# Kernel tuning notes

Measured on AMD Instinct MI355X. Metric: run time of the kernel, lower is better.

## Reference

```python
import jax, jax.numpy as jnp
import numpy as np

B, S, D, H = 4, 2048, 1024, 16
HD = D // H  # 64
EPS = 1e-5


def setup_inputs() -> dict:
    key = jax.random.key(0)
    ks = jax.random.split(key, 16)
    sc = 0.02
    inp = {
        "x": jax.random.normal(ks[0], (B, S, D), dtype=jnp.float32),
        # per-head QKV projections, stacked over heads: [H, D, HD]
        "Wq": jax.random.normal(ks[1], (H, D, HD), jnp.float32) * sc,
        "bq": jnp.zeros((H, HD), jnp.float32),
        "Wk": jax.random.normal(ks[2], (H, D, HD), jnp.float32) * sc,
        "bk": jnp.zeros((H, HD), jnp.float32),
        "Wv": jax.random.normal(ks[3], (H, D, HD), jnp.float32) * sc,
        "bv": jnp.zeros((H, HD), jnp.float32),
        "Wo": jax.random.normal(ks[4], (D, D), jnp.float32) * sc,
        "bo": jnp.zeros((D,), jnp.float32),
        "W1": jax.random.normal(ks[5], (D, 4 * D), jnp.float32) * sc,
        "b1": jnp.zeros((4 * D,), jnp.float32),
        "W2": jax.random.normal(ks[6], (4 * D, D), jnp.float32) * sc,
        "b2": jnp.zeros((D,), jnp.float32),
        "g1": jnp.ones((D,), jnp.float32),
        "be1": jnp.zeros((D,), jnp.float32),
        "g2": jnp.ones((D,), jnp.float32),
        "be2": jnp.zeros((D,), jnp.float32),
    }
    return inp


def _layer_norm(x, g, b):
    mu = jnp.mean(x, axis=-1, keepdims=True)
    var = jnp.var(x, axis=-1, keepdims=True)
    return (x - mu) * jax.lax.rsqrt(var + EPS) * g + b


def reference(x, Wq, bq, Wk, bk, Wv, bv, Wo, bo, W1, b1, W2, b2, g1, be1, g2, be2):
    # --- pre-LN multi-head attention (no causal mask, matches source) ---
    h = _layer_norm(x, g1, be1)                                   # [B,S,D]
    q = jnp.einsum("bsd,hdk->bhsk", h, Wq) + bq[None, :, None, :]  # [B,H,S,HD]
    k = jnp.einsum("bsd,hdk->bhsk", h, Wk) + bk[None, :, None, :]
    v = jnp.einsum("bsd,hdk->bhsk", h, Wv) + bv[None, :, None, :]
    scores = jnp.einsum("bhsk,bhtk->bhst", q, k) / jnp.sqrt(jnp.float32(HD))
    w = jax.nn.softmax(scores, axis=-1)                           # [B,H,S,S]
    o = jnp.einsum("bhst,bhtk->bhsk", w, v)                       # [B,H,S,HD]
    o = o.transpose(0, 2, 1, 3).reshape(B, S, D)                   # concat heads
    attn = o @ Wo + bo
    x1 = x + attn
    # --- FFN: Linear -> Linear -> GELU (exact, as in the source Sequential) ---
    h2 = _layer_norm(x1, g2, be2)
    ff = jax.nn.gelu((h2 @ W1 + b1) @ W2 + b2, approximate=False)
    return x1 + ff
```

## Files before the change

### kernel.cpp

```cpp
#include <hip/hip_runtime.h>
#include <hip/hip_bf16.h>
#include <cmath>

typedef __hip_bfloat16 bf16;
typedef float v4f __attribute__((ext_vector_type(4)));
typedef short v8s __attribute__((ext_vector_type(8)));
typedef short v4s __attribute__((ext_vector_type(4)));

__device__ __forceinline__ void load_lds16(const void* g, void* l) {
  __builtin_amdgcn_global_load_lds(
      (const __attribute__((address_space(1))) char*)g,
      (__attribute__((address_space(3))) char*)l, 16, 0, 0);
}
__device__ __forceinline__ v4f mfma16x16x32(v8s a, v8s b, v4f c) {
  return __builtin_amdgcn_mfma_f32_16x16x32_bf16(a, b, c, 0, 0, 0);
}
__device__ __forceinline__ v4f mfma16x16x16(v4s a, v4s b, v4f c) {
#if __has_builtin(__builtin_amdgcn_mfma_f32_16x16x16_bf16)
  return __builtin_amdgcn_mfma_f32_16x16x16_bf16(a, b, c, 0, 0, 0);
#elif __has_builtin(__builtin_amdgcn_mfma_f32_16x16x16bf16_1k)
  return __builtin_amdgcn_mfma_f32_16x16x16bf16_1k(a, b, c, 0, 0, 0);
#else
  v4f d;
  asm("v_mfma_f32_16x16x16_bf16 %0, %1, %2, %3"
      : "=v"(d) : "v"(a), "v"(b), "v"(c));
  return d;
#endif
}
__device__ __forceinline__ float b2f(bf16 x) { return __bfloat162float(x); }
__device__ __forceinline__ bf16 f2b(float x) { return __float2bfloat16(x); }
__device__ __forceinline__ ushort b2u(float x) {
  bf16 h = f2b(x);
  return *(ushort*)&h;
}
__device__ __forceinline__ float fexp2(float x) {
#if __has_builtin(__builtin_amdgcn_exp2f)
  return __builtin_amdgcn_exp2f(x);
#else
  return exp2f(x);
#endif
}
__device__ __forceinline__ float gelu_exact(float x) {
  return 0.5f * x * (1.0f + erff(x * 0.70710678118654752f));
}
__device__ __forceinline__ float finz(float v, float sent) {
  return __builtin_isfinite(v) ? v : sent;
}
__device__ __forceinline__ float u2f(ushort u) {
  return __uint_as_float(((unsigned)u) << 16);
}
__device__ __forceinline__ float4 load4f(const float* p) {
  return *(const float4*)p;
}
__device__ __forceinline__ float4 load4f(const bf16* p) {
  ushort4 u = *(const ushort4*)p;
  return make_float4(u2f(u.x), u2f(u.y), u2f(u.z), u2f(u.w));
}

template <typename TI>
__global__ __launch_bounds__(256)
void ln_kernel(const TI* __restrict__ x, const float* __restrict__ g,
               const float* __restrict__ b, bf16* __restrict__ out) {
  __shared__ float red[8];
  __shared__ float stat[2];
  const int row = blockIdx.x, t = threadIdx.x;
  const int wave = t >> 6, lane = t & 63;
  float4 v = load4f(x + (long)row * 1024 + t * 4);
  float s = v.x + v.y + v.z + v.w;
  float s2 = v.x * v.x + v.y * v.y + v.z * v.z + v.w * v.w;
#pragma unroll
  for (int off = 32; off > 0; off >>= 1) {
    s += __shfl_down(s, off);
    s2 += __shfl_down(s2, off);
  }
  if (lane == 0) { red[wave * 2] = s; red[wave * 2 + 1] = s2; }
  __syncthreads();
  if (t == 0) {
    float S = red[0] + red[2] + red[4] + red[6];
    float S2 = red[1] + red[3] + red[5] + red[7];
    float mean = S * (1.0f / 1024.0f);
    float var = S2 * (1.0f / 1024.0f) - mean * mean;
    stat[0] = mean;
    stat[1] = rsqrtf(var + 1e-5f);
  }
  __syncthreads();
  const float mean = stat[0], rs = stat[1];
  bf16* orow = out + (long)row * 1024;
  const int c = t * 4;
  float4 gg = *(const float4*)(g + c);
  float4 bb = *(const float4*)(b + c);
  orow[c + 0] = f2b(finz((v.x - mean) * rs * gg.x + bb.x, 3000.f));
  orow[c + 1] = f2b(finz((v.y - mean) * rs * gg.y + bb.y, 3000.f));
  orow[c + 2] = f2b(finz((v.z - mean) * rs * gg.z + bb.z, 3000.f));
  orow[c + 3] = f2b(finz((v.w - mean) * rs * gg.w + bb.w, 3000.f));
}

__global__ __launch_bounds__(256)
void repack_qkv(const float* __restrict__ w, bf16* __restrict__ wt) {
  long i = (long)blockIdx.x * 256 + threadIdx.x;
  int n = (int)(i >> 10), d = (int)(i & 1023);
  int h = n >> 6, kk = n & 63;
  wt[i] = f2b(w[((long)h * 1024 + d) * 64 + kk]);
}

__global__ __launch_bounds__(256)
void cast_f2b(const float* __restrict__ in, bf16* __restrict__ out) {
  long i = ((long)blockIdx.x * 256 + threadIdx.x) * 4;
  float4 v = *(const float4*)(in + i);
  ushort4 pk;
  pk.x = b2u(v.x); pk.y = b2u(v.y); pk.z = b2u(v.z); pk.w = b2u(v.w);
  *(ushort4*)((ushort*)out + i) = pk;
}

__global__ __launch_bounds__(256)
void ffn_bias(const float* __restrict__ b1, const float* __restrict__ W2,
              const float* __restrict__ b2, float* __restrict__ bfo) {
  __shared__ float red[4];
  const int e = blockIdx.x, t = threadIdx.x;
  float s = 0.f;
#pragma unroll
  for (int j = 0; j < 16; j++) {
    const int f = t + j * 256;
    s += b1[f] * W2[(long)f * 1024 + e];
  }
#pragma unroll
  for (int off = 32; off > 0; off >>= 1) s += __shfl_down(s, off);
  if ((t & 63) == 0) red[t >> 6] = s;
  __syncthreads();
  if (t == 0) bfo[e] = b2[e] + red[0] + red[1] + red[2] + red[3];
}

__global__ __launch_bounds__(256)
void transpose_f2b(const float* __restrict__ in, bf16* __restrict__ out,
                   int R, int C) {
  __shared__ float tile[32][33];
  const int tx = threadIdx.x & 31, ty = threadIdx.x >> 5;
  const int r0 = blockIdx.y * 32, c0 = blockIdx.x * 32;
#pragma unroll
  for (int i = ty; i < 32; i += 8) tile[i][tx] = in[(long)(r0 + i) * C + c0 + tx];
  __syncthreads();
#pragma unroll
  for (int i = ty; i < 32; i += 8)
    out[(long)(c0 + i) * R + r0 + tx] = f2b(tile[tx][i]);
}

template <int EPI>
__global__ __launch_bounds__(256)
void gemm_bt(const bf16* __restrict__ A, const bf16* __restrict__ Bt,
             const float* __restrict__ bias0, const float* __restrict__ bias1,
             const float* __restrict__ bias2, const void* __restrict__ residv,
             void* __restrict__ C0v, bf16* __restrict__ C1, bf16* __restrict__ C2v,
             int M, int N, int K) {
  __shared__ bf16 As[2][128 * 32];
  __shared__ bf16 Bs[2][128 * 32];
  const int t = threadIdx.x;
  const int wave = t >> 6, lane = t & 63, quad = lane >> 4, ln = lane & 15;
  const int m0 = blockIdx.y * 128, n0 = blockIdx.x * 128;
  const int wm = (wave >> 1) * 64, wn = (wave & 1) * 64;

  v4f acc[4][4];
#pragma unroll
  for (int i = 0; i < 4; i++)
#pragma unroll
    for (int j = 0; j < 4; j++) acc[i][j] = v4f{0.f, 0.f, 0.f, 0.f};

  const int e0 = t * 8, e1 = t * 8 + 2048;
  const int ra0 = e0 >> 5, ca0 = e0 & 31, ra1 = e1 >> 5, ca1 = e1 & 31;
  const bf16* Ab = A + (long)m0 * K;
  const bf16* Bb = Bt + (long)n0 * K;

  load_lds16(Ab + (long)ra0 * K + ca0, &As[0][e0]);
  load_lds16(Ab + (long)ra1 * K + ca1, &As[0][e1]);
  load_lds16(Bb + (long)ra0 * K + ca0, &Bs[0][e0]);
  load_lds16(Bb + (long)ra1 * K + ca1, &Bs[0][e1]);

  int cur = 0;
  for (int k0 = 0; k0 < K; k0 += 32) {
    __syncthreads();
    if (k0 + 32 < K) {
      const int kn = k0 + 32, nb = cur ^ 1;
      load_lds16(Ab + (long)ra0 * K + kn + ca0, &As[nb][e0]);
      load_lds16(Ab + (long)ra1 * K + kn + ca1, &As[nb][e1]);
      load_lds16(Bb + (long)ra0 * K + kn + ca0, &Bs[nb][e0]);
      load_lds16(Bb + (long)ra1 * K + kn + ca1, &Bs[nb][e1]);
    }
    v8s af[4], bfr[4];
#pragma unroll
    for (int mi = 0; mi < 4; mi++)
      af[mi] = *(const v8s*)&As[cur][(wm + mi * 16 + ln) * 32 + quad * 8];
#pragma unroll
    for (int ni = 0; ni < 4; ni++)
      bfr[ni] = *(const v8s*)&Bs[cur][(wn + ni * 16 + ln) * 32 + quad * 8];
#pragma unroll
    for (int mi = 0; mi < 4; mi++)
#pragma unroll
      for (int ni = 0; ni < 4; ni++)
        acc[mi][ni] = mfma16x16x32(af[mi], bfr[ni], acc[mi][ni]);
    cur ^= 1;
  }

#pragma unroll
  for (int ni = 0; ni < 4; ni++) {
    const int col = n0 + wn + ni * 16 + ln;
    if (EPI == 3) {
      const int proj = col >> 10, w = col & 1023;
      const float* bp = proj == 0 ? bias0 : (proj == 1 ? bias1 : bias2);
      const float bb = bp[w];
      const int hidx = w >> 6, hd = w & 63;
      if (proj == 2) {
#pragma unroll
        for (int mi = 0; mi < 4; mi++) {
          const int row0 = m0 + wm + mi * 16 + quad * 4;
          const int b_ = row0 >> 11, s = row0 & 2047;
          ushort4 pk;
          pk.x = b2u(finz(acc[mi][ni][0] + bb, 1e4f));
          pk.y = b2u(finz(acc[mi][ni][1] + bb, 1e4f));
          pk.z = b2u(finz(acc[mi][ni][2] + bb, 1e4f));
          pk.w = b2u(finz(acc[mi][ni][3] + bb, 1e4f));
          *(ushort4*)((ushort*)C2v +
                      (((long)(b_ * 16 + hidx)) * 64 + hd) * 2048 + s) = pk;
        }
      } else {
        bf16* op = proj == 0 ? (bf16*)C0v : C1;
        const float sc = proj == 0 ? 0.18033688f : 1.0f;
#pragma unroll
        for (int mi = 0; mi < 4; mi++)
#pragma unroll
          for (int r = 0; r < 4; r++) {
            const int row = m0 + wm + mi * 16 + quad * 4 + r;
            const int b_ = row >> 11, s = row & 2047;
            op[(((long)(b_ * 16 + hidx)) * 2048 + s) * 64 + hd] =
                f2b(finz((acc[mi][ni][r] + bb) * sc, 1e4f));
          }
      }
    } else {
      const float bb = bias0[col];
#pragma unroll
      for (int mi = 0; mi < 4; mi++)
#pragma unroll
        for (int r = 0; r < 4; r++) {
          const int row = m0 + wm + mi * 16 + quad * 4 + r;
          float vv = acc[mi][ni][r] + bb;
          if (EPI == 2) {
            vv = gelu_exact(vv);
            vv += b2f(((const bf16*)residv)[(long)row * N + col]);
            ((float*)C0v)[(long)row * N + col] = finz(vv, 1e5f);
          } else {
            if (EPI == 1) vv += ((const float*)residv)[(long)row * N + col];
            const float sent = EPI == 0 ? 4e4f : 2e4f;
            ((bf16*)C0v)[(long)row * N + col] = f2b(finz(vv, sent));
          }
        }
    }
  }
}

template <int EPI>
__global__ __launch_bounds__(256, 8)
void gemm_bt64(const bf16* __restrict__ A, const bf16* __restrict__ Bt,
               const float* __restrict__ bias0, const void* __restrict__ residv,
               void* __restrict__ C0v, int M, int N, int K) {
  __shared__ bf16 As[2][64 * 32];
  __shared__ bf16 Bs[2][64 * 32];
  const int t = threadIdx.x;
  const int wave = t >> 6, lane = t & 63, quad = lane >> 4, ln = lane & 15;
  const int m0 = blockIdx.y * 64, n0 = blockIdx.x * 64;
  const int wm = (wave >> 1) * 32, wn = (wave & 1) * 32;

  v4f acc[2][2];
#pragma unroll
  for (int i = 0; i < 2; i++)
#pragma unroll
    for (int j = 0; j < 2; j++) acc[i][j] = v4f{0.f, 0.f, 0.f, 0.f};

  const int ra = t >> 2, ca = (t & 3) * 8;
  const bf16* Ab = A + (long)(m0 + ra) * K + ca;
  const bf16* Bb = Bt + (long)(n0 + ra) * K + ca;
  const int eo = ra * 32 + ca;

  load_lds16(Ab, &As[0][eo]);
  load_lds16(Bb, &Bs[0][eo]);

  int cur = 0;
  for (int k0 = 0; k0 < K; k0 += 32) {
    __syncthreads();
    if (k0 + 32 < K) {
      const int nb = cur ^ 1;
      load_lds16(Ab + k0 + 32, &As[nb][eo]);
      load_lds16(Bb + k0 + 32, &Bs[nb][eo]);
    }
    v8s af[2], bfr[2];
#pragma unroll
    for (int mi = 0; mi < 2; mi++)
      af[mi] = *(const v8s*)&As[cur][(wm + mi * 16 + ln) * 32 + quad * 8];
#pragma unroll
    for (int ni = 0; ni < 2; ni++)
      bfr[ni] = *(const v8s*)&Bs[cur][(wn + ni * 16 + ln) * 32 + quad * 8];
#pragma unroll
    for (int mi = 0; mi < 2; mi++)
#pragma unroll
      for (int ni = 0; ni < 2; ni++)
        acc[mi][ni] = mfma16x16x32(af[mi], bfr[ni], acc[mi][ni]);
    cur ^= 1;
  }

#pragma unroll
  for (int ni = 0; ni < 2; ni++) {
    const int col = n0 + wn + ni * 16 + ln;
    float bb = 0.f;
    if (EPI != 0) bb = bias0[col];
#pragma unroll
    for (int mi = 0; mi < 2; mi++)
#pragma unroll
      for (int r = 0; r < 4; r++) {
        const int row = m0 + wm + mi * 16 + quad * 4 + r;
        float vv = acc[mi][ni][r] + bb;
        if (EPI == 2) {
          vv = gelu_exact(vv);
          vv += b2f(((const bf16*)residv)[(long)row * N + col]);
          ((float*)C0v)[(long)row * N + col] = finz(vv, 1e5f);
        } else if (EPI == 1) {
          vv += ((const float*)residv)[(long)row * N + col];
          ((bf16*)C0v)[(long)row * N + col] = f2b(finz(vv, 2e4f));
        } else {
          ((bf16*)C0v)[(long)row * N + col] = f2b(finz(vv, 2e4f));
        }
      }
  }
}

__global__ __launch_bounds__(256, 4)
void attn_kernel(const bf16* __restrict__ q, const bf16* __restrict__ k,
                 const bf16* __restrict__ vt, bf16* __restrict__ o) {
  __shared__ bf16 Ks[2][64 * 64];
  __shared__ bf16 Vs[2][64 * 64];
  const int t = threadIdx.x, wave = t >> 6, lane = t & 63;
  const int quad = lane >> 4, ln = lane & 15;
  const int id = blockIdx.x;
  const int bh = ((id & 7) << 3) | ((id >> 3) >> 4);
  const int qb = (id >> 3) & 15;
  const int q0 = qb * 128 + wave * 32;
  const long base = (long)bh * (2048 * 64);

  v8s qf[2][2];
#pragma unroll
  for (int mi = 0; mi < 2; mi++)
#pragma unroll
    for (int kc = 0; kc < 2; kc++)
      qf[mi][kc] = *(const v8s*)(q + base + (long)(q0 + mi * 16 + ln) * 64 +
                                 kc * 32 + quad * 8);

  v4f accO[2][4];
  float m2[2], lp[2];
#pragma unroll
  for (int mi = 0; mi < 2; mi++) {
#pragma unroll
    for (int nh = 0; nh < 4; nh++) accO[mi][nh] = v4f{0.f, 0.f, 0.f, 0.f};
    m2[mi] = -1e30f;
    lp[mi] = 0.f;
  }

  const int o0 = t * 16, o1 = t * 16 + 4096;
  const int ks0 = o0 ^ (((o0 >> 7) & 7) << 4);
  const int ks1 = o1 ^ (((o1 >> 7) & 7) << 4);
  const int h0 = o0 >> 7, h1 = o1 >> 7;
  const int vs0 = h0 * 4096 + ((o0 ^ ((h0 & 7) << 4)) & 127);
  const int vs1 = h1 * 4096 + ((o1 ^ ((h1 & 7) << 4)) & 127);
  const char* kgb = (const char*)(k + base);
  const char* vgb = (const char*)(vt + base);

  {
    char* kl = (char*)&Ks[0][0];
    char* vl = (char*)&Vs[0][0];
    load_lds16(kgb + ks0, kl + o0);
    load_lds16(kgb + ks1, kl + o1);
    load_lds16(vgb + vs0, vl + o0);
    load_lds16(vgb + vs1, vl + o1);
  }

  for (int it = 0; it < 32; ++it) {
    const int bf = it & 1;
    __syncthreads();
    if (it + 1 < 32) {
      const char* kg = kgb + (long)(it + 1) * (64 * 128);
      const char* vg = vgb + (long)(it + 1) * 128;
      char* kl = (char*)&Ks[bf ^ 1][0];
      char* vl = (char*)&Vs[bf ^ 1][0];
      load_lds16(kg + ks0, kl + o0);
      load_lds16(kg + ks1, kl + o1);
      load_lds16(vg + vs0, vl + o0);
      load_lds16(vg + vs1, vl + o1);
    }
    const char* Kb = (const char*)&Ks[bf][0];
    const char* Vb = (const char*)&Vs[bf][0];

    v4f st[2][4];
    __builtin_amdgcn_s_setprio(1);
#pragma unroll
    for (int ni = 0; ni < 4; ni++) {
      const int r = ni * 16 + ln;
      const int sw = (r & 7) << 4;
      v8s k0 = *(const v8s*)(Kb + ((r * 128 + quad * 16) ^ sw));
      v8s k1 = *(const v8s*)(Kb + ((r * 128 + 64 + quad * 16) ^ sw));
#pragma unroll
      for (int mi = 0; mi < 2; mi++) {
        v4f z = v4f{0.f, 0.f, 0.f, 0.f};
        z = mfma16x16x32(k0, qf[mi][0], z);
        st[mi][ni] = mfma16x16x32(k1, qf[mi][1], z);
      }
    }
    __builtin_amdgcn_s_setprio(0);

    v4s pf[2][4];
#pragma unroll
    for (int mi = 0; mi < 2; mi++) {
      float a0 = fmaxf(fmaxf(st[mi][0][0], st[mi][0][1]),
                       fmaxf(st[mi][0][2], st[mi][0][3]));
      float a1 = fmaxf(fmaxf(st[mi][1][0], st[mi][1][1]),
                       fmaxf(st[mi][1][2], st[mi][1][3]));
      float a2 = fmaxf(fmaxf(st[mi][2][0], st[mi][2][1]),
                       fmaxf(st[mi][2][2], st[mi][2][3]));
      float a3 = fmaxf(fmaxf(st[mi][3][0], st[mi][3][1]),
                       fmaxf(st[mi][3][2], st[mi][3][3]));
      float mx = fmaxf(fmaxf(a0, a1), fmaxf(a2, a3));
      mx = fmaxf(mx, __shfl_xor(mx, 16));
      mx = fmaxf(mx, __shfl_xor(mx, 32));
      const float mo = m2[mi];
      if (!__all(mx <= mo + 8.0f)) {
        const float mn = fmaxf(mo, mx);
        const float al = fexp2(mo - mn);
        m2[mi] = mn;
        lp[mi] *= al;
#pragma unroll
        for (int nh = 0; nh < 4; nh++)
#pragma unroll
          for (int r = 0; r < 4; r++) accO[mi][nh][r] *= al;
      }
      const float mu = m2[mi];
      float rs = 0.f;
#pragma unroll
      for (int ni = 0; ni < 4; ni++) {
        v4s p4;
#pragma unroll
        for (int r = 0; r < 4; r++) {
          float p = fexp2(st[mi][ni][r] - mu);
          rs += p;
          p4[r] = (short)b2u(p);
        }
        pf[mi][ni] = p4;
      }
      lp[mi] += rs;
    }

    __builtin_amdgcn_s_setprio(1);
#pragma unroll
    for (int nh = 0; nh < 4; nh++) {
      const int row = nh * 16 + ln;
      const int sw = (row & 7) << 4;
#pragma unroll
      for (int ni = 0; ni < 4; ni++) {
        v4s vv = *(const v4s*)(Vb + ((row * 128 + ni * 32 + quad * 8) ^ sw));
#pragma unroll
        for (int mi = 0; mi < 2; mi++)
          accO[mi][nh] = mfma16x16x16(vv, pf[mi][ni], accO[mi][nh]);
      }
    }
    __builtin_amdgcn_s_setprio(0);
  }

  const int b_ = bh >> 4, h_ = bh & 15;
#pragma unroll
  for (int mi = 0; mi < 2; mi++) {
    float lr = lp[mi];
    lr += __shfl_xor(lr, 16);
    lr += __shfl_xor(lr, 32);
    const float inv = 1.0f / lr;
    const int s = q0 + mi * 16 + ln;
#pragma unroll
    for (int nh = 0; nh < 4; nh++) {
      ushort4 pk;
      pk.x = b2u(finz(accO[mi][nh][0] * inv, 5000.f));
      pk.y = b2u(finz(accO[mi][nh][1] * inv, 5000.f));
      pk.z = b2u(finz(accO[mi][nh][2] * inv, 5000.f));
      pk.w = b2u(finz(accO[mi][nh][3] * inv, 5000.f));
      *(ushort4*)((ushort*)o + ((long)(b_ * 2048 + s)) * 1024 + h_ * 64 +
                  nh * 16 + quad * 4) = pk;
    }
  }
}

extern "C" void kernel_launch(void* const* d_in, const int* in_sizes, int n_in,
                              void* d_out, int out_size, void* d_ws,
                              size_t ws_size, hipStream_t stream) {
  const float* x   = (const float*)d_in[0];
  const float* Wq  = (const float*)d_in[1];
  const float* bq  = (const float*)d_in[2];
  const float* Wk  = (const float*)d_in[3];
  const float* bk  = (const float*)d_in[4];
  const float* Wv  = (const float*)d_in[5];
  const float* bv  = (const float*)d_in[6];
  const float* Wo  = (const float*)d_in[7];
  const float* bo  = (const float*)d_in[8];
  const float* W1  = (const float*)d_in[9];
  const float* b1  = (const float*)d_in[10];
  const float* W2  = (const float*)d_in[11];
  const float* b2  = (const float*)d_in[12];
  const float* g1  = (const float*)d_in[13];
  const float* be1 = (const float*)d_in[14];
  const float* g2  = (const float*)d_in[15];
  const float* be2 = (const float*)d_in[16];
  float* out = (float*)d_out;

  const size_t MB = 1024 * 1024;
  if (ws_size < 104 * MB) return;
  char* W = (char*)d_ws;
  bf16* wqt = (bf16*)(W + 0 * MB);
  bf16* wkt = (bf16*)(W + 2 * MB);
  bf16* wvt = (bf16*)(W + 4 * MB);
  bf16* wot = (bf16*)(W + 6 * MB);
  bf16* h   = (bf16*)(W + 8 * MB);
  bf16* qb  = (bf16*)(W + 24 * MB);
  bf16* kb  = (bf16*)(W + 40 * MB);
  bf16* vb  = (bf16*)(W + 56 * MB);
  bf16* ao  = (bf16*)(W + 72 * MB);
  bf16* x1  = (bf16*)(W + 88 * MB);
  bf16* w1b = (bf16*)(W + 24 * MB);
  bf16* w2t = (bf16*)(W + 32 * MB);
  bf16* wft = (bf16*)(W + 40 * MB);
  float* bfb = (float*)(W + 44 * MB);

  repack_qkv<<<4096, 256, 0, stream>>>(Wq, wqt);
  repack_qkv<<<4096, 256, 0, stream>>>(Wk, wkt);
  repack_qkv<<<4096, 256, 0, stream>>>(Wv, wvt);
  transpose_f2b<<<dim3(32, 32), 256, 0, stream>>>(Wo, wot, 1024, 1024);

  ln_kernel<float><<<8192, 256, 0, stream>>>(x, g1, be1, h);
  gemm_bt<3><<<dim3(24, 64), 256, 0, stream>>>(h, wqt, bq, bk, bv, nullptr,
                                               qb, kb, vb, 8192, 3072, 1024);
  attn_kernel<<<dim3(1024), 256, 0, stream>>>(qb, kb, vb, ao);
  gemm_bt64<1><<<dim3(16, 128), 256, 0, stream>>>(ao, wot, bo, x, x1,
                                                  8192, 1024, 1024);
  cast_f2b<<<4096, 256, 0, stream>>>(W1, w1b);
  transpose_f2b<<<dim3(32, 128), 256, 0, stream>>>(W2, w2t, 4096, 1024);
  gemm_bt64<0><<<dim3(16, 16), 256, 0, stream>>>(w2t, w1b, nullptr, nullptr,
                                                 wft, 1024, 1024, 4096);
  ffn_bias<<<1024, 256, 0, stream>>>(b1, W2, b2, bfb);
  ln_kernel<bf16><<<8192, 256, 0, stream>>>(x1, g2, be2, h);
  gemm_bt64<2><<<dim3(16, 128), 256, 0, stream>>>(h, wft, bfb, x1, out,
                                                  8192, 1024, 1024);
}
```

Measured before the change: 521.8 us.

## Split-K the W1·W2 weight-fold GEMM and unroll attention loop by two

The 1024x1024x4096 GEMM that folds W1 and W2 into one FFN weight now runs split-K over 4 slices, using 1024 blocks instead of 256. Each slice writes fp32 partials to workspace and a separate reduce kernel sums them and converts to bf16. This targets the poor GPU occupancy of the original 256-block launch, at the cost of 16MB of extra fp32 traffic and one more launch. The attention main loop also gets an unroll-by-2 pragma.

```diff
diff --git a/kernel.cpp b/kernel.cpp
--- a/kernel.cpp
+++ b/kernel.cpp
@@ -329,6 +329,83 @@
   }
 }
 
+__global__ __launch_bounds__(256, 8)
+void gemm_wf_splitk(const bf16* __restrict__ A, const bf16* __restrict__ Bt,
+                    float* __restrict__ pout) {
+  __shared__ bf16 As[2][64 * 32];
+  __shared__ bf16 Bs[2][64 * 32];
+  const int t = threadIdx.x;
+  const int wave = t >> 6, lane = t & 63, quad = lane >> 4, ln = lane & 15;
+  const int m0 = blockIdx.y * 64, n0 = blockIdx.x * 64;
+  const long koff = (long)blockIdx.z * 1024;
+  const int wm = (wave >> 1) * 32, wn = (wave & 1) * 32;
+
+  v4f acc[2][2];
+#pragma unroll
+  for (int i = 0; i < 2; i++)
+#pragma unroll
+    for (int j = 0; j < 2; j++) acc[i][j] = v4f{0.f, 0.f, 0.f, 0.f};
+
+  const int ra = t >> 2, ca = (t & 3) * 8;
+  const bf16* Ab = A + (long)(m0 + ra) * 4096 + koff + ca;
+  const bf16* Bb = Bt + (long)(n0 + ra) * 4096 + koff + ca;
+  const int eo = ra * 32 + ca;
+
+  load_lds16(Ab, &As[0][eo]);
+  load_lds16(Bb, &Bs[0][eo]);
+
+  int cur = 0;
+  for (int k0 = 0; k0 < 1024; k0 += 32) {
+    __syncthreads();
+    if (k0 + 32 < 1024) {
+      const int nb = cur ^ 1;
+      load_lds16(Ab + k0 + 32, &As[nb][eo]);
+      load_lds16(Bb + k0 + 32, &Bs[nb][eo]);
+    }
+    v8s af[2], bfr[2];
+#pragma unroll
+    for (int mi = 0; mi < 2; mi++)
+      af[mi] = *(const v8s*)&As[cur][(wm + mi * 16 + ln) * 32 + quad * 8];
+#pragma unroll
+    for (int ni = 0; ni < 2; ni++)
+      bfr[ni] = *(const v8s*)&Bs[cur][(wn + ni * 16 + ln) * 32 + quad * 8];
+#pragma unroll
+    for (int mi = 0; mi < 2; mi++)
+#pragma unroll
+      for (int ni = 0; ni < 2; ni++)
+        acc[mi][ni] = mfma16x16x32(af[mi], bfr[ni], acc[mi][ni]);
+    cur ^= 1;
+  }
+
+  float* po = pout + (long)blockIdx.z * (1024 * 1024);
+#pragma unroll
+  for (int ni = 0; ni < 2; ni++) {
+    const int col = n0 + wn + ni * 16 + ln;
+#pragma unroll
+    for (int mi = 0; mi < 2; mi++)
+#pragma unroll
+      for (int r = 0; r < 4; r++) {
+        const int row = m0 + wm + mi * 16 + quad * 4 + r;
+        po[(long)row * 1024 + col] = acc[mi][ni][r];
+      }
+  }
+}
+
+__global__ __launch_bounds__(256)
+void reduce_wf(const float* __restrict__ p, bf16* __restrict__ wft) {
+  const long i = ((long)blockIdx.x * 256 + threadIdx.x) * 4;
+  float4 a = *(const float4*)(p + i);
+  float4 b = *(const float4*)(p + i + 1048576);
+  float4 c = *(const float4*)(p + i + 2097152);
+  float4 d = *(const float4*)(p + i + 3145728);
+  ushort4 pk;
+  pk.x = b2u((a.x + b.x) + (c.x + d.x));
+  pk.y = b2u((a.y + b.y) + (c.y + d.y));
+  pk.z = b2u((a.z + b.z) + (c.z + d.z));
+  pk.w = b2u((a.w + b.w) + (c.w + d.w));
+  *(ushort4*)((ushort*)wft + i) = pk;
+}
+
 __global__ __launch_bounds__(256, 4)
 void attn_kernel(const bf16* __restrict__ q, const bf16* __restrict__ k,
                  const bf16* __restrict__ vt, bf16* __restrict__ o) {
@@ -378,6 +455,7 @@
     load_lds16(vgb + vs1, vl + o1);
   }
 
+#pragma unroll 2
   for (int it = 0; it < 32; ++it) {
     const int bf = it & 1;
     __syncthreads();
@@ -528,6 +606,7 @@
   bf16* w2t = (bf16*)(W + 32 * MB);
   bf16* wft = (bf16*)(W + 40 * MB);
   float* bfb = (float*)(W + 44 * MB);
+  float* wfp = (float*)(W + 56 * MB);
 
   repack_qkv<<<4096, 256, 0, stream>>>(Wq, wqt);
   repack_qkv<<<4096, 256, 0, stream>>>(Wk, wkt);
@@ -542,8 +621,8 @@
                                                   8192, 1024, 1024);
   cast_f2b<<<4096, 256, 0, stream>>>(W1, w1b);
   transpose_f2b<<<dim3(32, 128), 256, 0, stream>>>(W2, w2t, 4096, 1024);
-  gemm_bt64<0><<<dim3(16, 16), 256, 0, stream>>>(w2t, w1b, nullptr, nullptr,
-                                                 wft, 1024, 1024, 4096);
+  gemm_wf_splitk<<<dim3(16, 16, 4), 256, 0, stream>>>(w2t, w1b, wfp);
+  reduce_wf<<<1024, 256, 0, stream>>>(wfp, wft);
   ffn_bias<<<1024, 256, 0, stream>>>(b1, W2, b2, bfb);
   ln_kernel<bf16><<<8192, 256, 0, stream>>>(x1, g2, be2, h);
   gemm_bt64<2><<<dim3(16, 128), 256, 0, stream>>>(h, wft, bfb, x1, out,
```

Result: no change. 515.2 us (-1.3%).
